# Kernel optimization log

Hardware: AMD Instinct MI355X
Metric: run time of the kernel (lower is better)

Reference implementation:

```python
import jax, jax.numpy as jnp
import numpy as np

N_NODES = 100000


def _sage_conv(x, src, dst, W_l, b, W_r):
    """PyG SAGEConv with mean aggregation: lin_l(mean_{j in N(i)} x_j) + lin_r(x_i).
    edge_index[0]=src (message source j), edge_index[1]=dst (target i)."""
    n = x.shape[0]
    # sum of neighbor features per target node, then divide by in-degree
    agg = jax.ops.segment_sum(x[src], dst, num_segments=n)  # [N, F]
    deg = jax.ops.segment_sum(jnp.ones_like(dst, dtype=x.dtype), dst, num_segments=n)
    agg = agg / jnp.maximum(deg, 1.0)[:, None]
    return agg @ W_l + b + x @ W_r


def setup_inputs() -> dict:
    key = jax.random.key(0)
    ks = jax.random.split(key, 8)
    in_c, hid, out = 128, 128, 2
    sc = lambda f: 1.0 / np.sqrt(f)
    x = jax.random.normal(ks[0], (N_NODES, in_c), dtype=jnp.float32)
    edge_index = jax.random.randint(ks[1], (2, 1600000), 0, N_NODES, dtype=jnp.int64)
    return {
        "x": x,
        "edge_index": edge_index,
        "W1_l": jax.random.normal(ks[2], (in_c, hid), dtype=jnp.float32) * sc(in_c),
        "b1": jnp.zeros((hid,), dtype=jnp.float32),
        "W1_r": jax.random.normal(ks[3], (in_c, hid), dtype=jnp.float32) * sc(in_c),
        "W2_l": jax.random.normal(ks[4], (hid, hid), dtype=jnp.float32) * sc(hid),
        "b2": jnp.zeros((hid,), dtype=jnp.float32),
        "W2_r": jax.random.normal(ks[5], (hid, hid), dtype=jnp.float32) * sc(hid),
        "W_fc": jax.random.normal(ks[6], (hid, out), dtype=jnp.float32) * sc(hid),
        "b_fc": jnp.zeros((out,), dtype=jnp.float32),
    }


def reference(x, edge_index, W1_l, b1, W1_r, W2_l, b2, W2_r, W_fc, b_fc):
    src, dst = edge_index[0], edge_index[1]
    # eval mode: dropout is identity
    h = jax.nn.relu(_sage_conv(x, src, dst, W1_l, b1, W1_r))
    h = jax.nn.relu(_sage_conv(h, src, dst, W2_l, b2, W2_r))
    return h @ W_fc + b_fc
```

## Files before the change

kernel.cpp:

```cpp
#include <hip/hip_runtime.h>

#define NF 128
#define SH 9
#define BNODES 512
#define MAXNB 256

typedef unsigned short u16;
typedef unsigned int u32;
using u16x4 = __attribute__((ext_vector_type(4))) u16;
using u16x8 = __attribute__((ext_vector_type(8))) u16;
using s16x8 = __attribute__((ext_vector_type(8))) short;
using f32x4 = __attribute__((ext_vector_type(4))) float;
using u32x4 = __attribute__((ext_vector_type(4))) u32;
using i32x4 = __attribute__((ext_vector_type(4))) int;

__device__ inline float b2f(u16 b) {
    union { u32 u; float f; } c; c.u = (u32)b << 16; return c.f;
}
__device__ inline float lo2f(u32 w) {
    union { u32 u; float f; } c; c.u = w << 16; return c.f;
}
__device__ inline float hi2f(u32 w) {
    union { u32 u; float f; } c; c.u = w & 0xFFFF0000u; return c.f;
}
__device__ inline u16 f2b(float f) {
    union { float f; u32 u; } c; c.f = f;
    u32 u = c.u;
    u += 0x7FFFu + ((u >> 16) & 1u);
    return (u16)(u >> 16);
}
__device__ inline u16x8 nt_load8(const u16* p) {
    u32x4 v = __builtin_nontemporal_load((const u32x4*)p);
    return *(u16x8*)&v;
}
__device__ inline void nt_store8(u16* p, u16x8 v) {
    __builtin_nontemporal_store(*(u32x4*)&v, (u32x4*)p);
}
__device__ inline int padded4(int d) { return (d + 3) & ~3; }

__global__ __launch_bounds__(256) void bhist_kernel(const int* __restrict__ dst,
                                                    int* __restrict__ bcnt, int E, int NB) {
    __shared__ int h[MAXNB];
    int t = threadIdx.x;
    h[t] = 0;
    __syncthreads();
    for (int e = blockIdx.x * 256 + t; e < E; e += gridDim.x * 256)
        atomicAdd(&h[__builtin_nontemporal_load(dst + e) >> SH], 1);
    __syncthreads();
    if (t < NB && h[t]) atomicAdd(&bcnt[t], h[t]);
}

__global__ __launch_bounds__(256) void bscan_kernel(const int* __restrict__ bcnt,
                                                    int* __restrict__ boff,
                                                    int* __restrict__ gcur, int NB, int E) {
    __shared__ int ss[256];
    int t = threadIdx.x;
    int v = (t < NB) ? bcnt[t] : 0;
    ss[t] = v; __syncthreads();
    for (int off = 1; off < 256; off <<= 1) {
        int u = (t >= off) ? ss[t - off] : 0;
        __syncthreads();
        ss[t] += u;
        __syncthreads();
    }
    int excl = ss[t] - v;
    if (t < NB) { boff[t] = excl; gcur[t] = excl; }
    if (t == 0) boff[NB] = E;
}

__global__ __launch_bounds__(256) void scatter_kernel(
    const int* __restrict__ src, const int* __restrict__ dst,
    int* __restrict__ gcur, u32* __restrict__ pairs, int E, int NB)
{
    __shared__ int hist[MAXNB];
    __shared__ int cstart[256];
    __shared__ int gbase[MAXNB];
    __shared__ u32 stage[4096];
    __shared__ u16 bmap[4096];
    int t = threadIdx.x;
    int base = blockIdx.x * 4096;

    hist[t] = 0;
    __syncthreads();

    u32 packed[16]; int bb[16]; int loff[16];
    #pragma unroll
    for (int j = 0; j < 16; j++) {
        int e = base + j * 256 + t;
        bb[j] = -1;
        if (e < E) {
            int d = __builtin_nontemporal_load(dst + e);
            int s = __builtin_nontemporal_load(src + e);
            int b = d >> SH;
            bb[j] = b;
            packed[j] = ((u32)(d & (BNODES - 1)) << 17) | (u32)s;
            loff[j] = atomicAdd(&hist[b], 1);
        }
    }
    __syncthreads();

    int hv = hist[t];
    cstart[t] = hv; __syncthreads();
    for (int off = 1; off < 256; off <<= 1) {
        int u = (t >= off) ? cstart[t - off] : 0;
        __syncthreads();
        cstart[t] += u;
        __syncthreads();
    }
    int excl = cstart[t] - hv;
    if (t < NB && hv > 0) gbase[t] = atomicAdd(&gcur[t], hv);
    __syncthreads();
    cstart[t] = excl;
    __syncthreads();

    #pragma unroll
    for (int j = 0; j < 16; j++) if (bb[j] >= 0) {
        int pos = cstart[bb[j]] + loff[j];
        stage[pos] = packed[j];
        bmap[pos] = (u16)bb[j];
    }
    __syncthreads();

    int total = min(4096, E - base);
    for (int k = t; k < total; k += 256) {
        u32 p = stage[k];
        int b = bmap[k];
        pairs[gbase[b] + (k - cstart[b])] = p;
    }
}

__global__ __launch_bounds__(256) void degb_kernel(const u32* __restrict__ pairs,
                                                   const int* __restrict__ boff,
                                                   int* __restrict__ deg, int n) {
    __shared__ int dl[BNODES];
    int b = blockIdx.x, t = threadIdx.x;
    for (int i = t; i < BNODES; i += 256) dl[i] = 0;
    __syncthreads();
    int s = boff[b], e = boff[b + 1];
    for (int k = s + t; k < e; k += 256)
        atomicAdd(&dl[__builtin_nontemporal_load(pairs + k) >> 17], 1);
    __syncthreads();
    int nb0 = b << SH;
    for (int i = t; i < BNODES; i += 256)
        if (nb0 + i < n) deg[nb0 + i] = dl[i];
}

__global__ __launch_bounds__(256) void scanA_kernel(const int* __restrict__ deg,
                                                    int* __restrict__ bsum, int n) {
    __shared__ int red[256];
    int t = threadIdx.x;
    int i0 = blockIdx.x * 1024 + t * 4;
    int s = 0;
    if (i0 + 3 < n) {
        int4 d = *(const int4*)(deg + i0);
        s = padded4(d.x) + padded4(d.y) + padded4(d.z) + padded4(d.w);
    } else {
        for (int j = 0; j < 4; j++) if (i0 + j < n) s += padded4(deg[i0 + j]);
    }
    red[t] = s; __syncthreads();
    for (int off = 128; off; off >>= 1) {
        if (t < off) red[t] += red[t + off];
        __syncthreads();
    }
    if (!t) bsum[blockIdx.x] = red[0];
}

__global__ __launch_bounds__(128) void scanB_kernel(int* __restrict__ bsum, int nb) {
    __shared__ int ss[128];
    int t = threadIdx.x;
    int v = (t < nb) ? bsum[t] : 0;
    ss[t] = v; __syncthreads();
    for (int off = 1; off < 128; off <<= 1) {
        int u = (t >= off) ? ss[t - off] : 0;
        __syncthreads();
        ss[t] += u;
        __syncthreads();
    }
    if (t < nb) bsum[t] = ss[t] - v;
}

__global__ __launch_bounds__(256) void scanC_kernel(const int* __restrict__ deg,
                                                    const int* __restrict__ bsum,
                                                    int* __restrict__ info,
                                                    int* __restrict__ adj, int n) {
    __shared__ int ss[256];
    int t = threadIdx.x;
    int i0 = blockIdx.x * 1024 + t * 4;
    int4 d = make_int4(0, 0, 0, 0);
    if (i0 + 3 < n) d = *(const int4*)(deg + i0);
    else {
        if (i0     < n) d.x = deg[i0];
        if (i0 + 1 < n) d.y = deg[i0 + 1];
        if (i0 + 2 < n) d.z = deg[i0 + 2];
        if (i0 + 3 < n) d.w = deg[i0 + 3];
    }
    int px = padded4(d.x), py = padded4(d.y), pz = padded4(d.z), pw = padded4(d.w);
    int s = px + py + pz + pw;
    ss[t] = s; __syncthreads();
    for (int off = 1; off < 256; off <<= 1) {
        int u = (t >= off) ? ss[t - off] : 0;
        __syncthreads();
        ss[t] += u;
        __syncthreads();
    }
    int b0 = bsum[blockIdx.x] + ss[t] - s;
    int b1 = b0 + px, b2 = b1 + py, b3 = b2 + pz;
    if (i0 + 3 < n) {
        i32x4 w0 = {b0, d.x, b1, d.y};
        i32x4 w1 = {b2, d.z, b3, d.w};
        ((i32x4*)info)[i0 / 2]     = w0;
        ((i32x4*)info)[i0 / 2 + 1] = w1;
    } else {
        if (i0     < n) { info[2 * i0]     = b0; info[2 * i0 + 1] = d.x; }
        if (i0 + 1 < n) { info[2 * i0 + 2] = b1; info[2 * i0 + 3] = d.y; }
        if (i0 + 2 < n) { info[2 * i0 + 4] = b2; info[2 * i0 + 5] = d.z; }
        if (i0 + 3 < n) { info[2 * i0 + 6] = b3; info[2 * i0 + 7] = d.w; }
    }
    if (i0     < n) for (int p = d.x; p < px; p++) adj[b0 + p] = n;
    if (i0 + 1 < n) for (int p = d.y; p < py; p++) adj[b1 + p] = n;
    if (i0 + 2 < n) for (int p = d.z; p < pz; p++) adj[b2 + p] = n;
    if (i0 + 3 < n) for (int p = d.w; p < pw; p++) adj[b3 + p] = n;
}

__global__ __launch_bounds__(256) void fill2_kernel(const u32* __restrict__ pairs,
                                                    const int* __restrict__ boff,
                                                    const int* __restrict__ info,
                                                    int* __restrict__ adj, int n) {
    __shared__ int begl[BNODES];
    __shared__ int curl[BNODES];
    int b = blockIdx.x, t = threadIdx.x;
    int nb0 = b << SH;
    for (int i = t; i < BNODES; i += 256) {
        int nd = nb0 + i;
        if (nd < n) begl[i] = info[2 * nd];
        curl[i] = 0;
    }
    __syncthreads();
    int s = boff[b], e = boff[b + 1];
    for (int k = s + t; k < e; k += 256) {
        u32 p = __builtin_nontemporal_load(pairs + k);
        int ld = p >> 17, sr = p & 0x1FFFF;
        int pos = atomicAdd(&curl[ld], 1);
        adj[begl[ld] + pos] = sr;
    }
}

__global__ __launch_bounds__(256) void cast_x_kernel(const float* __restrict__ x,
                                                     u16* __restrict__ xb, int n, int nr) {
    int i = blockIdx.x * 256 + threadIdx.x;
    if (i >= nr * (NF / 8)) return;
    int node = i >> 4, ch = i & 15;
    u16x8 o = (u16x8)0;
    if (node < n) {
        const float* p = x + (size_t)node * NF + ch * 8;
        f32x4 v0 = __builtin_nontemporal_load((const f32x4*)p);
        f32x4 v1 = __builtin_nontemporal_load((const f32x4*)(p + 4));
        o[0] = f2b(v0[0]); o[1] = f2b(v0[1]); o[2] = f2b(v0[2]); o[3] = f2b(v0[3]);
        o[4] = f2b(v1[0]); o[5] = f2b(v1[1]); o[6] = f2b(v1[2]); o[7] = f2b(v1[3]);
    }
    *(u16x8*)(xb + (size_t)node * NF + ch * 8) = o;
}

__global__ void cast_wt_kernel(const float* __restrict__ w0, const float* __restrict__ w1,
                               const float* __restrict__ w2, const float* __restrict__ w3,
                               u16* __restrict__ o0, u16* __restrict__ o1,
                               u16* __restrict__ o2, u16* __restrict__ o3) {
    int m = blockIdx.y;
    const float* w = (m == 0) ? w0 : (m == 1) ? w1 : (m == 2) ? w2 : w3;
    u16* o = (m == 0) ? o0 : (m == 1) ? o1 : (m == 2) ? o2 : o3;
    int i = blockIdx.x * 256 + threadIdx.x;
    int k = i >> 7, nc = i & 127;
    o[nc * NF + k] = f2b(w[k * NF + nc]);
}

template <bool FC>
__global__ __launch_bounds__(512) void sage_fused_kernel(
    const u16* __restrict__ xin,
    const int* __restrict__ info,
    const int* __restrict__ adj,
    const u16* __restrict__ Wtl,
    const u16* __restrict__ Wtr,
    const float* __restrict__ bias,
    const float* __restrict__ Wfc,
    const float* __restrict__ bfc,
    u16* __restrict__ hout,
    float* __restrict__ out,
    int n)
{
    constexpr int MT = 128;
    constexpr int LDK = 136;
    __shared__ u16 A_s[MT][LDK];
    __shared__ u16 W_s[NF][LDK];

    int t = threadIdx.x;
    int node0 = blockIdx.x * MT;

    #pragma unroll
    for (int i = 0; i < 4; i++) {
        int idx = t + i * 512;
        int row = idx >> 4, ch = idx & 15;
        *(u16x8*)&W_s[row][ch * 8] = ((const u16x8*)Wtl)[row * 16 + ch];
    }

    {
        int grp = t >> 4, lane = t & 15;
        const char* xbase = (const char*)xin;
        u32 lo16 = (u32)lane * 16;

        for (int j = 0; j < 4; j++) {
            int m = grp * 4 + j;
            int node = node0 + m;
            float L[4] = {0.f, 0.f, 0.f, 0.f}, H[4] = {0.f, 0.f, 0.f, 0.f};
            int dg = 0;
            if (node < n) {
                int2 inf = *(const int2*)(info + 2 * node);
                dg = inf.y;
                const i32x4* ap = (const i32x4*)(adj + inf.x);
                int ng = (dg + 3) >> 2;

#define ROWU(nb) (*(const u32x4*)(xbase + (((u32)(nb) << 8) + lo16)))
#define ACC4(cur) { \
    u32x4 r0 = ROWU(cur[0]), r1 = ROWU(cur[1]), r2 = ROWU(cur[2]), r3 = ROWU(cur[3]); \
    _Pragma("unroll") \
    for (int k = 0; k < 4; k++) { \
        L[k] += (lo2f(r0[k]) + lo2f(r1[k])) + (lo2f(r2[k]) + lo2f(r3[k])); \
        H[k] += (hi2f(r0[k]) + hi2f(r1[k])) + (hi2f(r2[k]) + hi2f(r3[k])); \
    } }
                i32x4 ia, ib;
                if (ng >= 2) {
                    ia = __builtin_nontemporal_load(ap);
                    ib = __builtin_nontemporal_load(ap + 1);
                }
                int g = 0;
                while (g + 2 <= ng) {
                    i32x4 ca = ia, cb = ib;
                    g += 2;
                    if (g + 2 <= ng) {
                        ia = __builtin_nontemporal_load(ap + g);
                        ib = __builtin_nontemporal_load(ap + g + 1);
                    }
                    ACC4(ca);
                    ACC4(cb);
                }
                if (g < ng) {
                    i32x4 ca = __builtin_nontemporal_load(ap + g);
                    ACC4(ca);
                }
#undef ACC4
#undef ROWU
            }
            float invd = 1.0f / fmaxf((float)dg, 1.0f);
            u16x8 o;
            #pragma unroll
            for (int k = 0; k < 4; k++) {
                o[2 * k]     = f2b(L[k] * invd);
                o[2 * k + 1] = f2b(H[k] * invd);
            }
            *(u16x8*)&A_s[m][lane * 8] = o;
        }
    }
    __syncthreads();

    int l = t & 63;
    int lr = l & 15;
    int lko = (l >> 4) * 8;
    int m0 = (t >> 6) * 16;

    f32x4 acc[8];
    #pragma unroll
    for (int f = 0; f < 8; f++) acc[f] = (f32x4)0.f;

    #pragma unroll
    for (int ks = 0; ks < NF; ks += 32) {
        s16x8 a = *(const s16x8*)&A_s[m0 + lr][ks + lko];
        #pragma unroll
        for (int f = 0; f < 8; f++) {
            s16x8 b = *(const s16x8*)&W_s[f * 16 + lr][ks + lko];
            acc[f] = __builtin_amdgcn_mfma_f32_16x16x32_bf16(a, b, acc[f], 0, 0, 0);
        }
    }
    __syncthreads();

    #pragma unroll
    for (int i = 0; i < 4; i++) {
        int idx = t + i * 512;
        int row = idx >> 4, ch = idx & 15;
        *(u16x8*)&W_s[row][ch * 8] = ((const u16x8*)Wtr)[row * 16 + ch];
    }
    #pragma unroll
    for (int i = 0; i < 4; i++) {
        int idx = t + i * 512;
        int row = idx >> 4, ch = idx & 15;
        int node = node0 + row;
        u16x8 v = (u16x8)0;
        if (node < n) v = nt_load8(xin + (size_t)node * NF + ch * 8);
        *(u16x8*)&A_s[row][ch * 8] = v;
    }
    __syncthreads();

    #pragma unroll
    for (int ks = 0; ks < NF; ks += 32) {
        s16x8 a = *(const s16x8*)&A_s[m0 + lr][ks + lko];
        #pragma unroll
        for (int f = 0; f < 8; f++) {
            s16x8 b = *(const s16x8*)&W_s[f * 16 + lr][ks + lko];
            acc[f] = __builtin_amdgcn_mfma_f32_16x16x32_bf16(a, b, acc[f], 0, 0, 0);
        }
    }

    __syncthreads();
    int rowb = m0 + (l >> 4) * 4;
    #pragma unroll
    for (int f = 0; f < 8; f++) {
        float bc = bias[f * 16 + lr];
        #pragma unroll
        for (int r = 0; r < 4; r++) {
            float v = fmaxf(acc[f][r] + bc, 0.f);
            A_s[rowb + r][f * 16 + lr] = f2b(v);
        }
    }
    __syncthreads();

    if (!FC) {
        #pragma unroll
        for (int i = 0; i < 4; i++) {
            int idx = t + i * 512;
            int row = idx >> 4, ch = idx & 15;
            int node = node0 + row;
            if (node < n)
                nt_store8(hout + (size_t)node * NF + ch * 8, *(u16x8*)&A_s[row][ch * 8]);
            else if (node == n)
                nt_store8(hout + (size_t)node * NF + ch * 8, (u16x8)0);
        }
    } else {
        int g = t >> 5, lane = t & 31;
        float2 wfc[4];
        #pragma unroll
        for (int j = 0; j < 4; j++) wfc[j] = ((const float2*)Wfc)[lane * 4 + j];
        float bf0 = bfc[0], bf1 = bfc[1];
        for (int m8 = 0; m8 < 8; m8++) {
            int m = g * 8 + m8;
            float p0 = 0.f, p1 = 0.f;
            #pragma unroll
            for (int j = 0; j < 4; j++) {
                float h = b2f(A_s[m][lane * 4 + j]);
                p0 += h * wfc[j].x;
                p1 += h * wfc[j].y;
            }
            #pragma unroll
            for (int s = 16; s; s >>= 1) {
                p0 += __shfl_down(p0, s, 32);
                p1 += __shfl_down(p1, s, 32);
            }
            int node = node0 + m;
            if (lane == 0 && node < n)
                *(float2*)(out + (size_t)node * 2) = make_float2(p0 + bf0, p1 + bf1);
        }
    }
}

extern "C" void kernel_launch(void* const* d_in, const int* in_sizes, int n_in,
                              void* d_out, int out_size, void* d_ws, size_t ws_size,
                              hipStream_t stream) {
    const float* x   = (const float*)d_in[0];
    const int*   ei  = (const int*)d_in[1];
    const float* W1l = (const float*)d_in[2];
    const float* b1  = (const float*)d_in[3];
    const float* W1r = (const float*)d_in[4];
    const float* W2l = (const float*)d_in[5];
    const float* b2  = (const float*)d_in[6];
    const float* W2r = (const float*)d_in[7];
    const float* Wfc = (const float*)d_in[8];
    const float* bfc = (const float*)d_in[9];

    const int n = in_sizes[0] / NF;
    const int E = in_sizes[1] / 2;
    const int nr = n + 1;
    const int NB = (n + BNODES - 1) >> SH;
    const int* src = ei;
    const int* dst = ei + E;

    u16* xb     = (u16*)d_ws;
    u16* h1     = xb + (size_t)nr * NF;
    u16* Wt1l   = h1 + (size_t)nr * NF;
    u16* Wt1r   = Wt1l + NF * NF;
    u16* Wt2l   = Wt1r + NF * NF;
    u16* Wt2r   = Wt2l + NF * NF;
    int* adj    = (int*)(Wt2r + NF * NF);
    int* deg    = adj + ((size_t)E + 3 * (size_t)n);
    int* info   = deg + n;
    int* bsum   = info + 2 * (size_t)n;
    int* bcnt   = bsum + 128;
    int* gcur   = bcnt + 256;
    int* boff   = gcur + 256;
    u32* pairs  = (u32*)(boff + 257);

    (void)hipMemsetAsync(bcnt, 0, 512 * sizeof(int), stream);

    bhist_kernel<<<1024, 256, 0, stream>>>(dst, bcnt, E, NB);
    bscan_kernel<<<1, 256, 0, stream>>>(bcnt, boff, gcur, NB, E);
    scatter_kernel<<<(E + 4095) / 4096, 256, 0, stream>>>(src, dst, gcur, pairs, E, NB);
    degb_kernel<<<NB, 256, 0, stream>>>(pairs, boff, deg, n);

    int nbA = (n + 1023) / 1024;
    scanA_kernel<<<nbA, 256, 0, stream>>>(deg, bsum, n);
    scanB_kernel<<<1, 128, 0, stream>>>(bsum, nbA);
    scanC_kernel<<<nbA, 256, 0, stream>>>(deg, bsum, info, adj, n);
    fill2_kernel<<<NB, 256, 0, stream>>>(pairs, boff, info, adj, n);

    cast_x_kernel<<<(nr * (NF / 8) + 255) / 256, 256, 0, stream>>>(x, xb, n, nr);
    cast_wt_kernel<<<dim3(64, 4), 256, 0, stream>>>(W1l, W1r, W2l, W2r,
                                                    Wt1l, Wt1r, Wt2l, Wt2r);

    int fb = (nr + 127) / 128;
    sage_fused_kernel<false><<<fb, 512, 0, stream>>>(
        xb, info, adj, Wt1l, Wt1r, b1, nullptr, nullptr, h1, nullptr, n);
    sage_fused_kernel<true><<<fb, 512, 0, stream>>>(
        h1, info, adj, Wt2l, Wt2r, b2, Wfc, bfc, nullptr, (float*)d_out, n);
}
```

Measured before the change: 265.2 us.

## Fuse CSR build scans into degree and fill kernels, add dynamic row scheduling

The degree kernel now also produces per-bucket padded sums, and a single scan plus a fused fillC kernel replace the scanA/scanB/scanC/fill2 chain. That removes two launches and a separate pass over the degree array. In the fused SAGE kernel, aggregation rows are handed out to wavefronts through an LDS atomic counter instead of a fixed assignment, to balance uneven degrees. The self-feature and W_r loads are issued early into registers so they overlap with aggregation. The cost is higher register pressure and atomic contention on the shared counter.

```diff
diff --git a/kernel.cpp b/kernel.cpp
--- a/kernel.cpp
+++ b/kernel.cpp
@@ -66,6 +66,20 @@
     int excl = ss[t] - v;
     if (t < NB) { boff[t] = excl; gcur[t] = excl; }
     if (t == 0) boff[NB] = E;
+}
+
+__global__ __launch_bounds__(256) void scan_excl_kernel(int* __restrict__ a, int nb) {
+    __shared__ int ss[256];
+    int t = threadIdx.x;
+    int v = (t < nb) ? a[t] : 0;
+    ss[t] = v; __syncthreads();
+    for (int off = 1; off < 256; off <<= 1) {
+        int u = (t >= off) ? ss[t - off] : 0;
+        __syncthreads();
+        ss[t] += u;
+        __syncthreads();
+    }
+    if (t < nb) a[t] = ss[t] - v;
 }
 
 __global__ __launch_bounds__(256) void scatter_kernel(
@@ -131,8 +145,10 @@
 
 __global__ __launch_bounds__(256) void degb_kernel(const u32* __restrict__ pairs,
                                                    const int* __restrict__ boff,
-                                                   int* __restrict__ deg, int n) {
+                                                   int* __restrict__ deg,
+                                                   int* __restrict__ bsumB, int n) {
     __shared__ int dl[BNODES];
+    __shared__ int red[256];
     int b = blockIdx.x, t = threadIdx.x;
     for (int i = t; i < BNODES; i += 256) dl[i] = 0;
     __syncthreads();
@@ -141,61 +157,36 @@
         atomicAdd(&dl[__builtin_nontemporal_load(pairs + k) >> 17], 1);
     __syncthreads();
     int nb0 = b << SH;
-    for (int i = t; i < BNODES; i += 256)
-        if (nb0 + i < n) deg[nb0 + i] = dl[i];
-}
-
-__global__ __launch_bounds__(256) void scanA_kernel(const int* __restrict__ deg,
-                                                    int* __restrict__ bsum, int n) {
-    __shared__ int red[256];
-    int t = threadIdx.x;
-    int i0 = blockIdx.x * 1024 + t * 4;
-    int s = 0;
-    if (i0 + 3 < n) {
-        int4 d = *(const int4*)(deg + i0);
-        s = padded4(d.x) + padded4(d.y) + padded4(d.z) + padded4(d.w);
-    } else {
-        for (int j = 0; j < 4; j++) if (i0 + j < n) s += padded4(deg[i0 + j]);
-    }
-    red[t] = s; __syncthreads();
+    int ps = 0;
+    for (int i = t; i < BNODES; i += 256) {
+        int d = dl[i];
+        if (nb0 + i < n) { deg[nb0 + i] = d; ps += padded4(d); }
+    }
+    red[t] = ps; __syncthreads();
     for (int off = 128; off; off >>= 1) {
         if (t < off) red[t] += red[t + off];
         __syncthreads();
     }
-    if (!t) bsum[blockIdx.x] = red[0];
-}
-
-__global__ __launch_bounds__(128) void scanB_kernel(int* __restrict__ bsum, int nb) {
-    __shared__ int ss[128];
-    int t = threadIdx.x;
-    int v = (t < nb) ? bsum[t] : 0;
-    ss[t] = v; __syncthreads();
-    for (int off = 1; off < 128; off <<= 1) {
-        int u = (t >= off) ? ss[t - off] : 0;
-        __syncthreads();
-        ss[t] += u;
-        __syncthreads();
-    }
-    if (t < nb) bsum[t] = ss[t] - v;
-}
-
-__global__ __launch_bounds__(256) void scanC_kernel(const int* __restrict__ deg,
-                                                    const int* __restrict__ bsum,
+    if (!t) bsumB[b] = red[0];
+}
+
+__global__ __launch_bounds__(256) void fillC_kernel(const u32* __restrict__ pairs,
+                                                    const int* __restrict__ boff,
+                                                    const int* __restrict__ deg,
+                                                    const int* __restrict__ bbase,
                                                     int* __restrict__ info,
                                                     int* __restrict__ adj, int n) {
+    __shared__ int begl[BNODES];
+    __shared__ int curl[BNODES];
     __shared__ int ss[256];
-    int t = threadIdx.x;
-    int i0 = blockIdx.x * 1024 + t * 4;
-    int4 d = make_int4(0, 0, 0, 0);
-    if (i0 + 3 < n) d = *(const int4*)(deg + i0);
-    else {
-        if (i0     < n) d.x = deg[i0];
-        if (i0 + 1 < n) d.y = deg[i0 + 1];
-        if (i0 + 2 < n) d.z = deg[i0 + 2];
-        if (i0 + 3 < n) d.w = deg[i0 + 3];
-    }
-    int px = padded4(d.x), py = padded4(d.y), pz = padded4(d.z), pw = padded4(d.w);
-    int s = px + py + pz + pw;
+    int b = blockIdx.x, t = threadIdx.x;
+    int nb0 = b << SH;
+    int i0 = 2 * t, i1 = 2 * t + 1;
+    int d0 = 0, d1 = 0;
+    if (nb0 + i0 < n) d0 = deg[nb0 + i0];
+    if (nb0 + i1 < n) d1 = deg[nb0 + i1];
+    int p0 = padded4(d0), p1 = padded4(d1);
+    int s = p0 + p1;
     ss[t] = s; __syncthreads();
     for (int off = 1; off < 256; off <<= 1) {
         int u = (t >= off) ? ss[t - off] : 0;
@@ -203,41 +194,21 @@
         ss[t] += u;
         __syncthreads();
     }
-    int b0 = bsum[blockIdx.x] + ss[t] - s;
-    int b1 = b0 + px, b2 = b1 + py, b3 = b2 + pz;
-    if (i0 + 3 < n) {
-        i32x4 w0 = {b0, d.x, b1, d.y};
-        i32x4 w1 = {b2, d.z, b3, d.w};
-        ((i32x4*)info)[i0 / 2]     = w0;
-        ((i32x4*)info)[i0 / 2 + 1] = w1;
-    } else {
-        if (i0     < n) { info[2 * i0]     = b0; info[2 * i0 + 1] = d.x; }
-        if (i0 + 1 < n) { info[2 * i0 + 2] = b1; info[2 * i0 + 3] = d.y; }
-        if (i0 + 2 < n) { info[2 * i0 + 4] = b2; info[2 * i0 + 5] = d.z; }
-        if (i0 + 3 < n) { info[2 * i0 + 6] = b3; info[2 * i0 + 7] = d.w; }
-    }
-    if (i0     < n) for (int p = d.x; p < px; p++) adj[b0 + p] = n;
-    if (i0 + 1 < n) for (int p = d.y; p < py; p++) adj[b1 + p] = n;
-    if (i0 + 2 < n) for (int p = d.z; p < pz; p++) adj[b2 + p] = n;
-    if (i0 + 3 < n) for (int p = d.w; p < pw; p++) adj[b3 + p] = n;
-}
-
-__global__ __launch_bounds__(256) void fill2_kernel(const u32* __restrict__ pairs,
-                                                    const int* __restrict__ boff,
-                                                    const int* __restrict__ info,
-                                                    int* __restrict__ adj, int n) {
-    __shared__ int begl[BNODES];
-    __shared__ int curl[BNODES];
-    int b = blockIdx.x, t = threadIdx.x;
-    int nb0 = b << SH;
-    for (int i = t; i < BNODES; i += 256) {
-        int nd = nb0 + i;
-        if (nd < n) begl[i] = info[2 * nd];
-        curl[i] = 0;
-    }
-    __syncthreads();
-    int s = boff[b], e = boff[b + 1];
-    for (int k = s + t; k < e; k += 256) {
+    int beg0 = bbase[b] + ss[t] - s;
+    int beg1 = beg0 + p0;
+    if (nb0 + i1 < n) {
+        i32x4 w = {beg0, d0, beg1, d1};
+        ((i32x4*)info)[(nb0 >> 1) + t] = w;
+    } else if (nb0 + i0 < n) {
+        info[2 * (nb0 + i0)] = beg0; info[2 * (nb0 + i0) + 1] = d0;
+    }
+    begl[i0] = beg0; curl[i0] = 0;
+    begl[i1] = beg1; curl[i1] = 0;
+    if (nb0 + i0 < n) for (int p = d0; p < p0; p++) adj[beg0 + p] = n;
+    if (nb0 + i1 < n) for (int p = d1; p < p1; p++) adj[beg1 + p] = n;
+    __syncthreads();
+    int sE = boff[b], eE = boff[b + 1];
+    for (int k = sE + t; k < eE; k += 256) {
         u32 p = __builtin_nontemporal_load(pairs + k);
         int ld = p >> 17, sr = p & 0x1FFFF;
         int pos = atomicAdd(&curl[ld], 1);
@@ -291,24 +262,37 @@
     constexpr int LDK = 136;
     __shared__ u16 A_s[MT][LDK];
     __shared__ u16 W_s[NF][LDK];
+    __shared__ int curn;
 
     int t = threadIdx.x;
     int node0 = blockIdx.x * MT;
 
+    if (t == 0) curn = 0;
+
+    u16x8 wrv[4], selfv[4];
     #pragma unroll
     for (int i = 0; i < 4; i++) {
         int idx = t + i * 512;
         int row = idx >> 4, ch = idx & 15;
         *(u16x8*)&W_s[row][ch * 8] = ((const u16x8*)Wtl)[row * 16 + ch];
-    }
+        wrv[i] = ((const u16x8*)Wtr)[row * 16 + ch];
+        int node = node0 + row;
+        selfv[i] = (u16x8)0;
+        if (node < n) selfv[i] = nt_load8(xin + (size_t)node * NF + ch * 8);
+    }
+    __syncthreads();
 
     {
-        int grp = t >> 4, lane = t & 15;
+        int g4 = (t >> 4) & 3, lane = t & 15;
         const char* xbase = (const char*)xin;
         u32 lo16 = (u32)lane * 16;
 
-        for (int j = 0; j < 4; j++) {
-            int m = grp * 4 + j;
+        while (true) {
+            int grab = 0;
+            if ((t & 63) == 0) grab = atomicAdd(&curn, 4);
+            grab = __shfl(grab, 0, 64);
+            if (grab >= MT) break;
+            int m = grab + g4;
             int node = node0 + m;
             float L[4] = {0.f, 0.f, 0.f, 0.f}, H[4] = {0.f, 0.f, 0.f, 0.f};
             int dg = 0;
@@ -385,16 +369,8 @@
     for (int i = 0; i < 4; i++) {
         int idx = t + i * 512;
         int row = idx >> 4, ch = idx & 15;
-        *(u16x8*)&W_s[row][ch * 8] = ((const u16x8*)Wtr)[row * 16 + ch];
-    }
-    #pragma unroll
-    for (int i = 0; i < 4; i++) {
-        int idx = t + i * 512;
-        int row = idx >> 4, ch = idx & 15;
-        int node = node0 + row;
-        u16x8 v = (u16x8)0;
-        if (node < n) v = nt_load8(xin + (size_t)node * NF + ch * 8);
-        *(u16x8*)&A_s[row][ch * 8] = v;
+        *(u16x8*)&W_s[row][ch * 8] = wrv[i];
+        *(u16x8*)&A_s[row][ch * 8] = selfv[i];
     }
     __syncthreads();
 
@@ -489,8 +465,8 @@
     int* adj    = (int*)(Wt2r + NF * NF);
     int* deg    = adj + ((size_t)E + 3 * (size_t)n);
     int* info   = deg + n;
-    int* bsum   = info + 2 * (size_t)n;
-    int* bcnt   = bsum + 128;
+    int* bsumB  = info + 2 * (size_t)n;
+    int* bcnt   = bsumB + 256;
     int* gcur   = bcnt + 256;
     int* boff   = gcur + 256;
     u32* pairs  = (u32*)(boff + 257);
@@ -500,13 +476,9 @@
     bhist_kernel<<<1024, 256, 0, stream>>>(dst, bcnt, E, NB);
     bscan_kernel<<<1, 256, 0, stream>>>(bcnt, boff, gcur, NB, E);
     scatter_kernel<<<(E + 4095) / 4096, 256, 0, stream>>>(src, dst, gcur, pairs, E, NB);
-    degb_kernel<<<NB, 256, 0, stream>>>(pairs, boff, deg, n);
-
-    int nbA = (n + 1023) / 1024;
-    scanA_kernel<<<nbA, 256, 0, stream>>>(deg, bsum, n);
-    scanB_kernel<<<1, 128, 0, stream>>>(bsum, nbA);
-    scanC_kernel<<<nbA, 256, 0, stream>>>(deg, bsum, info, adj, n);
-    fill2_kernel<<<NB, 256, 0, stream>>>(pairs, boff, info, adj, n);
+    degb_kernel<<<NB, 256, 0, stream>>>(pairs, boff, deg, bsumB, n);
+    scan_excl_kernel<<<1, 256, 0, stream>>>(bsumB, NB);
+    fillC_kernel<<<NB, 256, 0, stream>>>(pairs, boff, deg, bsumB, info, adj, n);
 
     cast_x_kernel<<<(nr * (NF / 8) + 255) / 256, 256, 0, stream>>>(x, xb, n, nr);
     cast_wt_kernel<<<dim3(64, 4), 256, 0, stream>>>(W1l, W1r, W2l, W2r,
```

Result: slower. 283.1 us (+6.8%).
